# Performance work log

Hardware: AMD Instinct MI355X
Metric: run time of the kernel (lower is better)

## Reference

```python
import jax, jax.numpy as jnp
import numpy as np
from math import factorial, sqrt, pi

RS_IN = [(16, 0, 0), (16, 1, 0), (16, 2, 0)]
RS_OUT = [(16, 0, 0), (16, 1, 0), (16, 2, 0)]
HIDDEN = 100

def _l_filters(l_in, l_out):
    return list(range(abs(l_in - l_out), l_in + l_out + 1))

SET_L = sorted({l for _, li, _ in RS_IN for _, lo, _ in RS_OUT for l in _l_filters(li, lo)})
N_IN = sum(m * (2 * l + 1) for m, l, _ in RS_IN)
N_OUT = sum(m * (2 * l + 1) for m, l, _ in RS_OUT)
N_PATH = sum(mo * mi * len(_l_filters(li, lo)) for mo, lo, _ in RS_OUT for mi, li, _ in RS_IN)

def _cg_complex(j1, j2, j3):
    # Racah formula for SU(2) Clebsch-Gordan <j1 m1 j2 m2 | j3 m3> (integer l)
    f = lambda n: float(factorial(n))
    C = np.zeros((2 * j1 + 1, 2 * j2 + 1, 2 * j3 + 1))
    pref0 = sqrt((2 * j3 + 1) * f(j1 + j2 - j3) * f(j1 - j2 + j3) * f(-j1 + j2 + j3) / f(j1 + j2 + j3 + 1))
    for m1 in range(-j1, j1 + 1):
        for m2 in range(-j2, j2 + 1):
            m3 = m1 + m2
            if abs(m3) > j3:
                continue
            pref = pref0 * sqrt(f(j3 + m3) * f(j3 - m3) * f(j1 - m1) * f(j1 + m1) * f(j2 - m2) * f(j2 + m2))
            klo = max(0, j2 - j3 - m1, j1 + m2 - j3)
            khi = min(j1 + j2 - j3, j1 - m1, j2 + m2)
            s = 0.0
            for k in range(klo, khi + 1):
                s += (-1) ** k / (f(k) * f(j1 + j2 - j3 - k) * f(j1 - m1 - k) * f(j2 + m2 - k) * f(j3 - j2 + m1 + k) * f(j3 - j1 - m2 + k))
            C[j1 + m1, j2 + m2, j3 + m3] = pref * s
    return C

def _w3j(j1, j2, j3):
    cg = _cg_complex(j1, j2, j3)
    W = np.zeros_like(cg)
    for m3 in range(-j3, j3 + 1):
        W[:, :, j3 + m3] = (-1) ** (j1 - j2 + m3) / sqrt(2 * j3 + 1) * cg[:, :, j3 - m3]
    return W

def _Q(l):
    # complex -> real spherical-harmonic change of basis, rows m_real=-l..l, cols m=-l..l
    q = np.zeros((2 * l + 1, 2 * l + 1), dtype=complex)
    q[l, l] = 1.0
    s2 = 1.0 / sqrt(2.0)
    for m in range(1, l + 1):
        q[l + m, l + m] = (-1) ** m * s2
        q[l + m, l - m] = s2
        q[l - m, l - m] = 1j * s2
        q[l - m, l + m] = -1j * (-1) ** m * s2
    return q

def _real_cg(l1, l2, l3):
    # rotation-invariant 3-tensor in the real irrep basis, unit Frobenius norm (e3nn convention)
    c = np.einsum('am,bn,ck,mnk->abc', _Q(l1), _Q(l2), _Q(l3), _w3j(l1, l2, l3).astype(complex))
    re, im = np.real(c), np.imag(c)
    c = re if np.linalg.norm(re) >= np.linalg.norm(im) else im
    return jnp.asarray((c / np.linalg.norm(c)).astype(np.float32))

_CG = {}
for _mo, _lo, _ in RS_OUT:
    for _mi, _li, _ in RS_IN:
        for _lf in _l_filters(_li, _lo):
            if (_lo, _li, _lf) not in _CG:
                _CG[(_lo, _li, _lf)] = _real_cg(_lo, _li, _lf)

def _norm_coef():
    nc = np.zeros((len(RS_OUT), len(RS_IN), 2), dtype=np.float32)
    for i, (mul_out, l_out, _) in enumerate(RS_OUT):
        num = sum(mi * len(_l_filters(li, l_out)) for mi, li, _ in RS_IN)
        for j, (mul_in, l_in, _) in enumerate(RS_IN):
            lm = sqrt(2 * l_in + 1) * sqrt(4 * pi)  # normalization='norm'
            nc[i, j, 0] = lm / sqrt(num)
            nc[i, j, 1] = lm / sqrt(mul_in)
    return jnp.asarray(nc)

NORM_COEF = _norm_coef()

def _sh(u):
    # u: [B,3] unit vectors -> [25,B] real orthonormal SH, l=0..4, m=-l..l
    x, y, z = u[:, 0], u[:, 1], u[:, 2]
    x2, y2, z2 = x * x, y * y, z * z
    ys = [
        jnp.full_like(x, 0.5 * sqrt(1 / pi)),
        sqrt(3 / (4 * pi)) * y, sqrt(3 / (4 * pi)) * z, sqrt(3 / (4 * pi)) * x,
        0.5 * sqrt(15 / pi) * x * y, 0.5 * sqrt(15 / pi) * y * z, 0.25 * sqrt(5 / pi) * (3 * z2 - 1),
        0.5 * sqrt(15 / pi) * x * z, 0.25 * sqrt(15 / pi) * (x2 - y2),
        0.25 * sqrt(35 / (2 * pi)) * y * (3 * x2 - y2), 0.5 * sqrt(105 / pi) * x * y * z,
        0.25 * sqrt(21 / (2 * pi)) * y * (5 * z2 - 1), 0.25 * sqrt(7 / pi) * z * (5 * z2 - 3),
        0.25 * sqrt(21 / (2 * pi)) * x * (5 * z2 - 1), 0.25 * sqrt(105 / pi) * (x2 - y2) * z,
        0.25 * sqrt(35 / (2 * pi)) * x * (x2 - 3 * y2),
        0.75 * sqrt(35 / pi) * x * y * (x2 - y2), 0.75 * sqrt(35 / (2 * pi)) * y * (3 * x2 - y2) * z,
        0.75 * sqrt(5 / pi) * x * y * (7 * z2 - 1), 0.75 * sqrt(5 / (2 * pi)) * y * z * (7 * z2 - 3),
        (3.0 / 16.0) * sqrt(1 / pi) * (35 * z2 * z2 - 30 * z2 + 3),
        0.75 * sqrt(5 / (2 * pi)) * x * z * (7 * z2 - 3), (3.0 / 8.0) * sqrt(5 / pi) * (x2 - y2) * (7 * z2 - 1),
        0.75 * sqrt(35 / (2 * pi)) * x * (x2 - 3 * y2) * z,
        (3.0 / 16.0) * sqrt(35 / pi) * (x2 * x2 - 6 * x2 * y2 + y2 * y2),
    ]
    return jnp.stack(ys, axis=0)

def _kernel_forward(r, W1, b1, W2):
    size = r.shape[:-1]
    r2 = r.reshape(-1, 3)
    radii = jnp.linalg.norm(r2, axis=1)                      # [B]
    u = r2 / jnp.maximum(radii, 1e-12)[:, None]
    Ys = _sh(u)                                              # [25, B]
    h = jax.nn.relu(radii[:, None] * W1[0] + b1)             # radial MLP: [B,H]
    coeff = h @ W2                                           # [B, N_PATH]
    is_zero = radii == 0
    begin_c = 0
    rows = []
    for i, (mul_out, l_out, _) in enumerate(RS_OUT):
        row = []
        for j, (mul_in, l_in, _) in enumerate(RS_IN):
            lfs = _l_filters(l_in, l_out)
            n = mul_out * mul_in * len(lfs)
            c = coeff[:, begin_c:begin_c + n].reshape(-1, mul_out, mul_in, len(lfs))
            begin_c += n
            K = 0
            for k, lf in enumerate(lfs):
                off = sum(2 * l + 1 for l in SET_L if l < lf)
                Y = Ys[off:off + 2 * lf + 1]                 # [2lf+1, B]
                C = _CG[(l_out, l_in, lf)]                   # [2lo+1, 2li+1, 2lf+1]
                K = K + jnp.einsum('ijk,kz,zuv->zuivj', C, Y, c[..., k])
            norm = jnp.where(is_zero, NORM_COEF[i, j, 1], NORM_COEF[i, j, 0])
            K = K * norm[:, None, None, None, None]
            row.append(K.reshape(-1, mul_out * (2 * l_out + 1), mul_in * (2 * l_in + 1)))
        rows.append(jnp.concatenate(row, axis=2))
    kernel = jnp.concatenate(rows, axis=1)                   # [B, N_OUT, N_IN]
    return kernel.reshape(*size, N_OUT, N_IN)

def setup_inputs() -> dict:
    key = jax.random.key(0)
    k1, k2, k3, k4 = jax.random.split(key, 4)
    B = 8192
    return {
        'r': jax.random.normal(k1, (B, 3), dtype=jnp.float32),
        'W1': jax.random.normal(k2, (1, HIDDEN), dtype=jnp.float32),
        'b1': jax.random.normal(k3, (HIDDEN,), dtype=jnp.float32) * 0.1,
        'W2': jax.random.normal(k4, (HIDDEN, N_PATH), dtype=jnp.float32) / sqrt(HIDDEN),
    }

def reference(r, W1, b1, W2):
    return _kernel_forward(r, W1, b1, W2)
```

## Files before the change

### kernel.cpp

```cpp
#include <hip/hip_runtime.h>

#define NB     8192
#define NPB    3
#define NPATH  4864
#define NHID   100
#define NROW   144
#define NYSH   25
#define ND     259

__device__ unsigned short g_w2[NHID * NPATH];
__device__ float          g_cg[1225];

__device__ inline double dfact(int n) {
    const double F[13] = {1., 1., 2., 6., 24., 120., 720., 5040., 40320.,
                          362880., 3628800., 39916800., 479001600.};
    return F[n];
}

__device__ double cgc(int j1, int j2, int j3, int m1, int m2, int m3) {
    if (m1 + m2 != m3) return 0.0;
    double pref0 = sqrt((2 * j3 + 1) * dfact(j1 + j2 - j3) * dfact(j1 - j2 + j3) *
                        dfact(-j1 + j2 + j3) / dfact(j1 + j2 + j3 + 1));
    double pref = pref0 * sqrt(dfact(j3 + m3) * dfact(j3 - m3) * dfact(j1 - m1) *
                               dfact(j1 + m1) * dfact(j2 - m2) * dfact(j2 + m2));
    int klo = max(0, max(j2 - j3 - m1, j1 + m2 - j3));
    int khi = min(j1 + j2 - j3, min(j1 - m1, j2 + m2));
    double s = 0.0;
    for (int k = klo; k <= khi; k++) {
        double d = dfact(k) * dfact(j1 + j2 - j3 - k) * dfact(j1 - m1 - k) *
                   dfact(j2 + m2 - k) * dfact(j3 - j2 + m1 + k) * dfact(j3 - j1 - m2 + k);
        s += ((k & 1) ? -1.0 : 1.0) / d;
    }
    return pref * s;
}

__device__ double w3jf(int j1, int j2, int j3, int m1, int m2, int m3) {
    int e = j1 - j2 + m3;
    double sgn = (e & 1) ? -1.0 : 1.0;
    return sgn / sqrt((double)(2 * j3 + 1)) * cgc(j1, j2, j3, m1, m2, -m3);
}

__device__ int qrow(int l, int a, int* col, double* re, double* im) {
    const double s2 = 0.70710678118654752440;
    int m = a - l;
    if (m == 0) { col[0] = l; re[0] = 1.0; im[0] = 0.0; return 1; }
    if (m > 0) {
        col[0] = l + m; re[0] = (m & 1) ? -s2 : s2; im[0] = 0.0;
        col[1] = l - m; re[1] = s2;                 im[1] = 0.0;
        return 2;
    }
    int mm = -m;
    col[0] = l - mm; re[0] = 0.0; im[0] = s2;
    col[1] = l + mm; re[1] = 0.0; im[1] = (mm & 1) ? s2 : -s2;
    return 2;
}

__global__ void setup_kernel(const float* __restrict__ W2) {
    const int tid = threadIdx.x;
    const int bid = blockIdx.x;
    if (bid >= 19) {
        int idx = (bid - 19) * 256 + tid;
        if (idx < NHID * NPATH) {
            unsigned int u = __float_as_uint(W2[idx]);
            unsigned int r = (u + 0x7fffu + ((u >> 16) & 1u)) >> 16;
            g_w2[idx] = (unsigned short)r;
        }
        return;
    }
    const int TLO[19]  = {0,0,0,1,1,1,1,1,1,1,2,2,2,2,2,2,2,2,2};
    const int TLI[19]  = {0,1,2,0,1,1,1,2,2,2,0,1,1,1,2,2,2,2,2};
    const int TLF[19]  = {0,1,2,1,0,1,2,1,2,3,2,1,2,3,0,1,2,3,4};
    const int TOFF[19] = {0,1,10,35,44,53,80,125,170,245,350,375,420,495,600,625,700,825,1000};
    const int lo = TLO[bid], li = TLI[bid], lf = TLF[bid];
    const int n1 = 2 * lo + 1, n2 = 2 * li + 1, n3 = 2 * lf + 1;
    const int E = n1 * n2 * n3;

    __shared__ double sre[256], sim[256];
    __shared__ double snorm;
    __shared__ int ssel;

    double vre = 0.0, vim = 0.0;
    if (tid < E) {
        int g = tid % n3; int ab = tid / n3; int b = ab % n2; int a = ab / n2;
        int ca[2], cb[2], cc[2];
        double ra[2], ia[2], rb[2], ib[2], rc[2], ic[2];
        int na = qrow(lo, a, ca, ra, ia);
        int nb = qrow(li, b, cb, rb, ib);
        int nc = qrow(lf, g, cc, rc, ic);
        for (int p = 0; p < na; p++)
            for (int q = 0; q < nb; q++) {
                double pr = ra[p] * rb[q] - ia[p] * ib[q];
                double pi = ra[p] * ib[q] + ia[p] * rb[q];
                for (int s = 0; s < nc; s++) {
                    double w = w3jf(lo, li, lf, ca[p] - lo, cb[q] - li, cc[s] - lf);
                    if (w == 0.0) continue;
                    vre += (pr * rc[s] - pi * ic[s]) * w;
                    vim += (pr * ic[s] + pi * rc[s]) * w;
                }
            }
    }
    sre[tid] = vre * vre;
    sim[tid] = vim * vim;
    __syncthreads();
    if (tid == 0) {
        double sr = 0.0, si = 0.0;
        for (int e = 0; e < E; e++) { sr += sre[e]; si += sim[e]; }
        sr = sqrt(sr); si = sqrt(si);
        ssel = (sr >= si) ? 0 : 1;
        snorm = ssel ? si : sr;
    }
    __syncthreads();
    if (tid < E) {
        double val = ssel ? vim : vre;
        g_cg[TOFF[bid] + tid] = (float)(val / snorm);
    }
}

template <int LO, int LI, int NLF, int CB, int DB, int RB, int CO, int NUM>
__device__ __forceinline__ void expand_pair(const float* __restrict__ C,
                                            const float* __restrict__ D,
                                            float* __restrict__ op,
                                            int u, int v, bool zero) {
    constexpr int NO = 2 * LO + 1, NI = 2 * LI + 1;
    const float PI4 = 12.566370614359172f;
    const float n0 = sqrtf((2 * LI + 1) * PI4 / (float)NUM);
    const float n1 = sqrtf((2 * LI + 1) * PI4) * 0.25f;
    const float norm = zero ? n1 : n0;
    float c[NLF];
#pragma unroll
    for (int k = 0; k < NLF; k++) c[k] = norm * C[CB + (u * 16 + v) * NLF + k];
    const float* Dp = D + DB;
    float* o = op + (RB + u * NO) * NROW + CO + v * NI;
#pragma unroll
    for (int io = 0; io < NO; io++) {
#pragma unroll
        for (int jo = 0; jo < NI; jo++) {
            float s = 0.0f;
#pragma unroll
            for (int k = 0; k < NLF; k++) s += Dp[(io * NI + jo) * NLF + k] * c[k];
            o[io * NROW + jo] = s;
        }
    }
}

__global__ __launch_bounds__(256, 2) void tfn_kernel(const float* __restrict__ r,
                                                     const float* __restrict__ W1,
                                                     const float* __restrict__ b1,
                                                     float* __restrict__ out) {
    __shared__ float sC[NPB][NPATH];
    __shared__ float sY[NPB][NYSH];
    __shared__ float sH[NPB][NHID];
    __shared__ float sD[NPB][ND];
    __shared__ float sRad[NPB];
    __shared__ int   sZero[NPB];

    const int tid = threadIdx.x;
    const int zbase = blockIdx.x * NPB;

    if (tid < NPB) {
        int z = zbase + tid;
        float* Y = sY[tid];
        if (z < NB) {
            float x = r[3 * z], y = r[3 * z + 1], zc = r[3 * z + 2];
            float rad = sqrtf(x * x + y * y + zc * zc);
            sRad[tid] = rad;
            sZero[tid] = (rad == 0.0f) ? 1 : 0;
            float inv = 1.0f / fmaxf(rad, 1e-12f);
            x *= inv; y *= inv; zc *= inv;
            float x2 = x * x, y2 = y * y, z2 = zc * zc;
            Y[0] = 0.28209479177387814f;
            Y[1] = 0.4886025119029199f * y;
            Y[2] = 0.4886025119029199f * zc;
            Y[3] = 0.4886025119029199f * x;
            Y[4] = 1.0925484305920792f * x * y;
            Y[5] = 1.0925484305920792f * y * zc;
            Y[6] = 0.31539156525252005f * (3.0f * z2 - 1.0f);
            Y[7] = 1.0925484305920792f * x * zc;
            Y[8] = 0.5462742152960396f * (x2 - y2);
            Y[9]  = 0.5900435899266435f * y * (3.0f * x2 - y2);
            Y[10] = 2.890611442640554f * x * y * zc;
            Y[11] = 0.4570457994644658f * y * (5.0f * z2 - 1.0f);
            Y[12] = 0.3731763325901154f * zc * (5.0f * z2 - 3.0f);
            Y[13] = 0.4570457994644658f * x * (5.0f * z2 - 1.0f);
            Y[14] = 1.445305721320277f * (x2 - y2) * zc;
            Y[15] = 0.5900435899266435f * x * (x2 - 3.0f * y2);
            Y[16] = 2.5033429417967046f * x * y * (x2 - y2);
            Y[17] = 1.7701307697799304f * y * (3.0f * x2 - y2) * zc;
            Y[18] = 0.9461746957575601f * x * y * (7.0f * z2 - 1.0f);
            Y[19] = 0.6690465435572892f * y * zc * (7.0f * z2 - 3.0f);
            Y[20] = 0.10578554691520431f * (35.0f * z2 * z2 - 30.0f * z2 + 3.0f);
            Y[21] = 0.6690465435572892f * x * zc * (7.0f * z2 - 3.0f);
            Y[22] = 0.47308734787878004f * (x2 - y2) * (7.0f * z2 - 1.0f);
            Y[23] = 1.7701307697799304f * x * (x2 - 3.0f * y2) * zc;
            Y[24] = 0.6258357354491761f * (x2 * x2 - 6.0f * x2 * y2 + y2 * y2);
        } else {
            sRad[tid] = 0.0f; sZero[tid] = 0;
            for (int i = 0; i < NYSH; i++) Y[i] = 0.0f;
        }
    }
    __syncthreads();

    for (int idx = tid; idx < NPB * NHID; idx += 256) {
        int zz = idx / NHID, i = idx - zz * NHID;
        sH[zz][i] = fmaxf(sRad[zz] * W1[i] + b1[i], 0.0f);
    }

    {
        const int dbase[10] = {0, 1, 4, 9, 12, 39, 84, 89, 134, 259};
        const int pnlf[9]   = {1, 1, 1, 1, 3, 3, 1, 3, 5};
        const int plf0[9]   = {0, 1, 2, 1, 0, 1, 2, 1, 0};
        const int ptab0[9]  = {0, 1, 2, 3, 4, 7, 10, 11, 14};
        const int toff[19]  = {0,1,10,35,44,53,80,125,170,245,350,375,420,495,600,625,700,825,1000};
        for (int idx = tid; idx < NPB * ND; idx += 256) {
            int zz = idx / ND, e = idx - zz * ND;
            int pp = 8;
            while (e < dbase[pp]) pp--;
            int le = e - dbase[pp];
            int nlf = pnlf[pp];
            int rr = le / nlf, k = le - rr * nlf;
            int lf = plf0[pp] + k, nf = 2 * lf + 1;
            const float* cg = &g_cg[toff[ptab0[pp] + k] + rr * nf];
            const float* Yp = &sY[zz][lf * lf];
            float s = 0.0f;
            for (int m = 0; m < nf; m++) s += cg[m] * Yp[m];
            sD[zz][e] = s;
        }
    }
    __syncthreads();

    {
        float acc0[19], acc1[19], acc2[19];
#pragma unroll
        for (int k = 0; k < 19; k++) { acc0[k] = 0.0f; acc1[k] = 0.0f; acc2[k] = 0.0f; }
        const unsigned int* w2u = (const unsigned int*)g_w2;
        for (int i = 0; i < NHID; i++) {
            float h0 = sH[0][i], h1 = sH[1][i], h2 = sH[2][i];
            const unsigned int* row = w2u + i * (NPATH / 2);
#pragma unroll
            for (int k = 0; k < 9; k++) {
                unsigned int w = row[tid + 256 * k];
                float wl = __uint_as_float(w << 16);
                float wh = __uint_as_float(w & 0xffff0000u);
                acc0[2 * k]     += h0 * wl; acc0[2 * k + 1] += h0 * wh;
                acc1[2 * k]     += h1 * wl; acc1[2 * k + 1] += h1 * wh;
                acc2[2 * k]     += h2 * wl; acc2[2 * k + 1] += h2 * wh;
            }
            unsigned short wt = g_w2[i * NPATH + 4608 + tid];
            float wf = __uint_as_float(((unsigned int)wt) << 16);
            acc0[18] += h0 * wf; acc1[18] += h1 * wf; acc2[18] += h2 * wf;
        }
#pragma unroll
        for (int k = 0; k < 9; k++) {
            int p = 2 * tid + 512 * k;
            *(float2*)&sC[0][p] = make_float2(acc0[2 * k], acc0[2 * k + 1]);
            *(float2*)&sC[1][p] = make_float2(acc1[2 * k], acc1[2 * k + 1]);
            *(float2*)&sC[2][p] = make_float2(acc2[2 * k], acc2[2 * k + 1]);
        }
        sC[0][4608 + tid] = acc0[18];
        sC[1][4608 + tid] = acc1[18];
        sC[2][4608 + tid] = acc2[18];
    }
    __syncthreads();

    const int u = tid >> 4, v = tid & 15;
    for (int zz = 0; zz < NPB; zz++) {
        int z = zbase + zz;
        if (z >= NB) break;
        float* op = out + (size_t)z * (NROW * NROW);
        bool zero = (sZero[zz] != 0);
        const float* C = sC[zz];
        const float* D = sD[zz];
        expand_pair<0, 0, 1,    0,    0,   0,  0,  48 >(C, D, op, u, v, zero);
        expand_pair<0, 1, 1,  256,    1,   0, 16,  48 >(C, D, op, u, v, zero);
        expand_pair<0, 2, 1,  512,    4,   0, 64,  48 >(C, D, op, u, v, zero);
        expand_pair<1, 0, 1,  768,    9,  16,  0, 112 >(C, D, op, u, v, zero);
        expand_pair<1, 1, 3, 1024,   12,  16, 16, 112 >(C, D, op, u, v, zero);
        expand_pair<1, 2, 3, 1792,   39,  16, 64, 112 >(C, D, op, u, v, zero);
        expand_pair<2, 0, 1, 2560,   84,  64,  0, 144 >(C, D, op, u, v, zero);
        expand_pair<2, 1, 3, 2816,   89,  64, 16, 144 >(C, D, op, u, v, zero);
        expand_pair<2, 2, 5, 3584,  134,  64, 64, 144 >(C, D, op, u, v, zero);
    }
}

extern "C" void kernel_launch(void* const* d_in, const int* in_sizes, int n_in,
                              void* d_out, int out_size, void* d_ws, size_t ws_size,
                              hipStream_t stream) {
    const float* r  = (const float*)d_in[0];
    const float* W1 = (const float*)d_in[1];
    const float* b1 = (const float*)d_in[2];
    const float* W2 = (const float*)d_in[3];
    float* out = (float*)d_out;

    setup_kernel<<<19 + (NHID * NPATH + 255) / 256, 256, 0, stream>>>(W2);

    const int nblocks = (NB + NPB - 1) / NPB;
    tfn_kernel<<<nblocks, 256, 0, stream>>>(r, W1, b1, out);
}
```

Measured before the change: 918.5 us.

## Permute W2 so each thread owns its (u,v) paths and keep coefficients in registers

The setup kernel now reorders the bf16 W2 so that the 19 path weights a thread needs for its (u,v) pair sit contiguously, padded to 24 entries. The main kernel loads them with wide vector loads and keeps the radial coefficients in registers instead of staging them through a 58 KB shared buffer with a barrier. Dropping that shared array lowers LDS use, and the launch bounds are raised to allow 4 blocks per CU. The trade-off is higher register pressure from 57 live accumulators plus a 19-entry weight array, and the padding adds some extra weight memory traffic.

```diff
diff --git a/kernel.cpp b/kernel.cpp
--- a/kernel.cpp
+++ b/kernel.cpp
@@ -8,8 +8,8 @@
 #define NYSH   25
 #define ND     259
 
-__device__ unsigned short g_w2[NHID * NPATH];
-__device__ float          g_cg[1225];
+__device__ __align__(16) unsigned short g_w2r[NHID * 256 * 24];
+__device__ float g_cg[1225];
 
 __device__ inline double dfact(int n) {
     const double F[13] = {1., 1., 2., 6., 24., 120., 720., 5040., 40320.,
@@ -60,10 +60,18 @@
     const int bid = blockIdx.x;
     if (bid >= 19) {
         int idx = (bid - 19) * 256 + tid;
-        if (idx < NHID * NPATH) {
-            unsigned int u = __float_as_uint(W2[idx]);
+        if (idx < NHID * 256 * 19) {
+            const int CBJ[19]  = {0, 256, 512, 768, 1024, 1024, 1024, 1792, 1792, 1792,
+                                  2560, 2816, 2816, 2816, 3584, 3584, 3584, 3584, 3584};
+            const int NLFJ[19] = {1, 1, 1, 1, 3, 3, 3, 3, 3, 3, 1, 3, 3, 3, 5, 5, 5, 5, 5};
+            const int KJ[19]   = {0, 0, 0, 0, 0, 1, 2, 0, 1, 2, 0, 0, 1, 2, 0, 1, 2, 3, 4};
+            int j = idx % 19;
+            int t = (idx / 19) & 255;
+            int i = idx / (19 * 256);
+            int p = CBJ[j] + t * NLFJ[j] + KJ[j];
+            unsigned int u = __float_as_uint(W2[i * NPATH + p]);
             unsigned int r = (u + 0x7fffu + ((u >> 16) & 1u)) >> 16;
-            g_w2[idx] = (unsigned short)r;
+            g_w2r[(i * 256 + t) * 24 + j] = (unsigned short)r;
         }
         return;
     }
@@ -116,8 +124,8 @@
     }
 }
 
-template <int LO, int LI, int NLF, int CB, int DB, int RB, int CO, int NUM>
-__device__ __forceinline__ void expand_pair(const float* __restrict__ C,
+template <int LO, int LI, int NLF, int CIDX, int DB, int RB, int CO, int NUM>
+__device__ __forceinline__ void expand_pair(const float (&A)[19],
                                             const float* __restrict__ D,
                                             float* __restrict__ op,
                                             int u, int v, bool zero) {
@@ -128,7 +136,7 @@
     const float norm = zero ? n1 : n0;
     float c[NLF];
 #pragma unroll
-    for (int k = 0; k < NLF; k++) c[k] = norm * C[CB + (u * 16 + v) * NLF + k];
+    for (int k = 0; k < NLF; k++) c[k] = norm * A[CIDX + k];
     const float* Dp = D + DB;
     float* o = op + (RB + u * NO) * NROW + CO + v * NI;
 #pragma unroll
@@ -143,13 +151,15 @@
     }
 }
 
-__global__ __launch_bounds__(256, 2) void tfn_kernel(const float* __restrict__ r,
+#define BF16LO(u) __uint_as_float((u) << 16)
+#define BF16HI(u) __uint_as_float((u) & 0xffff0000u)
+
+__global__ __launch_bounds__(256, 4) void tfn_kernel(const float* __restrict__ r,
                                                      const float* __restrict__ W1,
                                                      const float* __restrict__ b1,
                                                      float* __restrict__ out) {
-    __shared__ float sC[NPB][NPATH];
     __shared__ float sY[NPB][NYSH];
-    __shared__ float sH[NPB][NHID];
+    __shared__ float sHT[NHID][4];
     __shared__ float sD[NPB][ND];
     __shared__ float sRad[NPB];
     __shared__ int   sZero[NPB];
@@ -202,7 +212,7 @@
 
     for (int idx = tid; idx < NPB * NHID; idx += 256) {
         int zz = idx / NHID, i = idx - zz * NHID;
-        sH[zz][i] = fmaxf(sRad[zz] * W1[i] + b1[i], 0.0f);
+        sHT[i][zz] = fmaxf(sRad[zz] * W1[i] + b1[i], 0.0f);
     }
 
     {
@@ -228,57 +238,56 @@
     }
     __syncthreads();
 
+    float acc[NPB][19];
+#pragma unroll
+    for (int zz = 0; zz < NPB; zz++)
+#pragma unroll
+        for (int j = 0; j < 19; j++) acc[zz][j] = 0.0f;
     {
-        float acc0[19], acc1[19], acc2[19];
-#pragma unroll
-        for (int k = 0; k < 19; k++) { acc0[k] = 0.0f; acc1[k] = 0.0f; acc2[k] = 0.0f; }
-        const unsigned int* w2u = (const unsigned int*)g_w2;
+        const unsigned int* wp = (const unsigned int*)g_w2r + tid * 12;
         for (int i = 0; i < NHID; i++) {
-            float h0 = sH[0][i], h1 = sH[1][i], h2 = sH[2][i];
-            const unsigned int* row = w2u + i * (NPATH / 2);
-#pragma unroll
-            for (int k = 0; k < 9; k++) {
-                unsigned int w = row[tid + 256 * k];
-                float wl = __uint_as_float(w << 16);
-                float wh = __uint_as_float(w & 0xffff0000u);
-                acc0[2 * k]     += h0 * wl; acc0[2 * k + 1] += h0 * wh;
-                acc1[2 * k]     += h1 * wl; acc1[2 * k + 1] += h1 * wh;
-                acc2[2 * k]     += h2 * wl; acc2[2 * k + 1] += h2 * wh;
+            uint4 a  = *(const uint4*)(wp);
+            uint4 b  = *(const uint4*)(wp + 4);
+            uint2 c2 = *(const uint2*)(wp + 8);
+            wp += 256 * 12;
+            float4 h4 = *(const float4*)(&sHT[i][0]);
+            float w[19];
+            w[0]  = BF16LO(a.x);  w[1]  = BF16HI(a.x);
+            w[2]  = BF16LO(a.y);  w[3]  = BF16HI(a.y);
+            w[4]  = BF16LO(a.z);  w[5]  = BF16HI(a.z);
+            w[6]  = BF16LO(a.w);  w[7]  = BF16HI(a.w);
+            w[8]  = BF16LO(b.x);  w[9]  = BF16HI(b.x);
+            w[10] = BF16LO(b.y);  w[11] = BF16HI(b.y);
+            w[12] = BF16LO(b.z);  w[13] = BF16HI(b.z);
+            w[14] = BF16LO(b.w);  w[15] = BF16HI(b.w);
+            w[16] = BF16LO(c2.x); w[17] = BF16HI(c2.x);
+            w[18] = BF16LO(c2.y);
+#pragma unroll
+            for (int j = 0; j < 19; j++) {
+                acc[0][j] += h4.x * w[j];
+                acc[1][j] += h4.y * w[j];
+                acc[2][j] += h4.z * w[j];
             }
-            unsigned short wt = g_w2[i * NPATH + 4608 + tid];
-            float wf = __uint_as_float(((unsigned int)wt) << 16);
-            acc0[18] += h0 * wf; acc1[18] += h1 * wf; acc2[18] += h2 * wf;
-        }
-#pragma unroll
-        for (int k = 0; k < 9; k++) {
-            int p = 2 * tid + 512 * k;
-            *(float2*)&sC[0][p] = make_float2(acc0[2 * k], acc0[2 * k + 1]);
-            *(float2*)&sC[1][p] = make_float2(acc1[2 * k], acc1[2 * k + 1]);
-            *(float2*)&sC[2][p] = make_float2(acc2[2 * k], acc2[2 * k + 1]);
-        }
-        sC[0][4608 + tid] = acc0[18];
-        sC[1][4608 + tid] = acc1[18];
-        sC[2][4608 + tid] = acc2[18];
-    }
-    __syncthreads();
+        }
+    }
 
     const int u = tid >> 4, v = tid & 15;
+#pragma unroll
     for (int zz = 0; zz < NPB; zz++) {
         int z = zbase + zz;
         if (z >= NB) break;
         float* op = out + (size_t)z * (NROW * NROW);
         bool zero = (sZero[zz] != 0);
-        const float* C = sC[zz];
         const float* D = sD[zz];
-        expand_pair<0, 0, 1,    0,    0,   0,  0,  48 >(C, D, op, u, v, zero);
-        expand_pair<0, 1, 1,  256,    1,   0, 16,  48 >(C, D, op, u, v, zero);
-        expand_pair<0, 2, 1,  512,    4,   0, 64,  48 >(C, D, op, u, v, zero);
-        expand_pair<1, 0, 1,  768,    9,  16,  0, 112 >(C, D, op, u, v, zero);
-        expand_pair<1, 1, 3, 1024,   12,  16, 16, 112 >(C, D, op, u, v, zero);
-        expand_pair<1, 2, 3, 1792,   39,  16, 64, 112 >(C, D, op, u, v, zero);
-        expand_pair<2, 0, 1, 2560,   84,  64,  0, 144 >(C, D, op, u, v, zero);
-        expand_pair<2, 1, 3, 2816,   89,  64, 16, 144 >(C, D, op, u, v, zero);
-        expand_pair<2, 2, 5, 3584,  134,  64, 64, 144 >(C, D, op, u, v, zero);
+        expand_pair<0, 0, 1,  0,     0,   0,  0,  48 >(acc[zz], D, op, u, v, zero);
+        expand_pair<0, 1, 1,  1,     1,   0, 16,  48 >(acc[zz], D, op, u, v, zero);
+        expand_pair<0, 2, 1,  2,     4,   0, 64,  48 >(acc[zz], D, op, u, v, zero);
+        expand_pair<1, 0, 1,  3,     9,  16,  0, 112 >(acc[zz], D, op, u, v, zero);
+        expand_pair<1, 1, 3,  4,    12,  16, 16, 112 >(acc[zz], D, op, u, v, zero);
+        expand_pair<1, 2, 3,  7,    39,  16, 64, 112 >(acc[zz], D, op, u, v, zero);
+        expand_pair<2, 0, 1, 10,    84,  64,  0, 144 >(acc[zz], D, op, u, v, zero);
+        expand_pair<2, 1, 3, 11,    89,  64, 16, 144 >(acc[zz], D, op, u, v, zero);
+        expand_pair<2, 2, 5, 14,   134,  64, 64, 144 >(acc[zz], D, op, u, v, zero);
     }
 }
 
@@ -291,7 +300,7 @@
     const float* W2 = (const float*)d_in[3];
     float* out = (float*)d_out;
 
-    setup_kernel<<<19 + (NHID * NPATH + 255) / 256, 256, 0, stream>>>(W2);
+    setup_kernel<<<19 + (NHID * 256 * 19 + 255) / 256, 256, 0, stream>>>(W2);
 
     const int nblocks = (NB + NPB - 1) / NPB;
     tfn_kernel<<<nblocks, 256, 0, stream>>>(r, W1, b1, out);
```

Result: faster. 836.7 us (-8.9%).
